# Kernel optimization log

Measured on AMD Instinct MI355X. Metric: run time of the kernel, lower is better.

## Reference

```python
import jax, jax.numpy as jnp
import numpy as np

B, D, N, H = 2, 8, 40, 128
HID = 4 * H  # 512, MLP hidden width


def setup_inputs() -> dict:
    key = jax.random.key(0)
    ks = jax.random.split(key, 12)
    s_in = 1.0 / np.sqrt(2 * H)
    s_hid = 1.0 / np.sqrt(HID)
    return {
        "node_feature": jax.random.normal(ks[0], (B, D, N, H), jnp.float32),
        "pairwise_feature": jax.random.normal(ks[1], (B, D, N, N, H), jnp.float32),
        # first MLP layer weight [2H, HID] split into node half and pairwise half
        "W1n": jax.random.uniform(ks[2], (H, HID), jnp.float32, -s_in, s_in),
        "W1p": jax.random.uniform(ks[3], (H, HID), jnp.float32, -s_in, s_in),
        "b1": jax.random.uniform(ks[4], (HID,), jnp.float32, -s_in, s_in),
        "W2": jax.random.uniform(ks[5], (HID, HID), jnp.float32, -s_hid, s_hid),
        "b2": jax.random.uniform(ks[6], (HID,), jnp.float32, -s_hid, s_hid),
        "W3": jax.random.uniform(ks[7], (HID, 1), jnp.float32, -s_hid, s_hid),
        "b3": jax.random.uniform(ks[8], (1,), jnp.float32, -s_hid, s_hid),
        "scale": jnp.float32(1.0),
        "bias": jnp.float32(0.0),
    }


def reference(node_feature, pairwise_feature, W1n, W1p, b1, W2, b2, W3, b3, scale, bias):
    # max over the dataset axis
    nf = jnp.max(node_feature, axis=-3)        # [B, N, H]
    pf = jnp.max(pairwise_feature, axis=-4)    # [B, N, N, H]
    # First linear on concat([node_expand, pair_expand]) decomposed into two
    # small projections + broadcast add (mathematically identical to
    # Linear(concat) since W1 = [W1n; W1p]).
    hn = nf @ W1n                               # [B, N, HID]
    hp = pf @ W1p                               # [B, N, N, HID]
    h = jax.nn.relu(hn[:, :, None, None, :] + hp[:, None, :, :, :] + b1)  # [B,N,N,N,HID]
    h = jax.nn.relu(h @ W2 + b2)                # [B, N, N, N, HID]
    v = h @ W3 + b3                             # [B, N, N, N, 1]
    return jax.nn.sigmoid(scale * v + bias).squeeze(-1)  # [B, N, N, N]
```

## Files before the change

kernel.cpp:

```cpp
#include <hip/hip_runtime.h>
#include <math.h>

#define BB 2
#define DD 8
#define NN 40
#define HH 128
#define HID 512
#define NJK 1600
#define MROW 64000

typedef __attribute__((ext_vector_type(8))) short short8;
typedef __attribute__((ext_vector_type(4))) float floatx4;

static __device__ __forceinline__ unsigned short f2bf(float x) {
    unsigned int b = __float_as_uint(x);
    b += 0x7fffu + ((b >> 16) & 1u);
    return (unsigned short)(b >> 16);
}

__global__ __launch_bounds__(256) void prep_kernel(
        const float* __restrict__ node, const float* __restrict__ pair,
        const float* __restrict__ W1n, const float* __restrict__ W1p,
        const float* __restrict__ b1, const float* __restrict__ W2,
        float* __restrict__ hp, float* __restrict__ hnb,
        unsigned short* __restrict__ w2f) {
    const int bid = blockIdx.x;
    const int t = threadIdx.x;

    if (bid < 200) {
        __shared__ float pf[16][HH];
        const int rowbase = bid * 16;
        for (int e = t; e < 16*HH; e += 256) {
            int r16 = e >> 7, c = e & 127;
            int grow = rowbase + r16;
            int b = grow / NJK, jk = grow - b*NJK;
            float m = -INFINITY;
            #pragma unroll
            for (int d = 0; d < DD; ++d)
                m = fmaxf(m, pair[((size_t)((b*DD + d)*NJK + jk))*HH + c]);
            pf[r16][c] = m;
        }
        __syncthreads();
        const int rg = t >> 7, c4 = (t & 127) * 4;
        float4 acc[8];
        #pragma unroll
        for (int r = 0; r < 8; ++r) acc[r] = make_float4(0.f,0.f,0.f,0.f);
        #pragma unroll 4
        for (int h = 0; h < HH; ++h) {
            float4 wv = *(const float4*)&W1p[h*HID + c4];
            #pragma unroll
            for (int r = 0; r < 8; ++r) {
                float pv = pf[rg*8 + r][h];
                acc[r].x = fmaf(pv, wv.x, acc[r].x);
                acc[r].y = fmaf(pv, wv.y, acc[r].y);
                acc[r].z = fmaf(pv, wv.z, acc[r].z);
                acc[r].w = fmaf(pv, wv.w, acc[r].w);
            }
        }
        #pragma unroll
        for (int r = 0; r < 8; ++r)
            *(float4*)&hp[(size_t)(rowbase + rg*8 + r)*HID + c4] = acc[r];
    } else if (bid < 205) {
        __shared__ float nf[16][HH];
        const int rowbase = (bid - 200) * 16;
        for (int e = t; e < 16*HH; e += 256) {
            int r16 = e >> 7, c = e & 127;
            int grow = rowbase + r16;
            int b = grow / NN, i = grow - b*NN;
            float m = -INFINITY;
            #pragma unroll
            for (int d = 0; d < DD; ++d)
                m = fmaxf(m, node[((size_t)((b*DD + d)*NN + i))*HH + c]);
            nf[r16][c] = m;
        }
        __syncthreads();
        const int rg = t >> 7, c4 = (t & 127) * 4;
        float4 acc[8];
        #pragma unroll
        for (int r = 0; r < 8; ++r) acc[r] = make_float4(0.f,0.f,0.f,0.f);
        #pragma unroll 4
        for (int h = 0; h < HH; ++h) {
            float4 wv = *(const float4*)&W1n[h*HID + c4];
            #pragma unroll
            for (int r = 0; r < 8; ++r) {
                float nv = nf[rg*8 + r][h];
                acc[r].x = fmaf(nv, wv.x, acc[r].x);
                acc[r].y = fmaf(nv, wv.y, acc[r].y);
                acc[r].z = fmaf(nv, wv.z, acc[r].z);
                acc[r].w = fmaf(nv, wv.w, acc[r].w);
            }
        }
        float4 b1v = *(const float4*)&b1[c4];
        #pragma unroll
        for (int r = 0; r < 8; ++r) {
            float4 o = make_float4(acc[r].x + b1v.x, acc[r].y + b1v.y,
                                   acc[r].z + b1v.z, acc[r].w + b1v.w);
            *(float4*)&hnb[(size_t)(rowbase + rg*8 + r)*HID + c4] = o;
        }
    } else {
        int tid = (bid - 205)*256 + t;
        int frag = tid >> 6;
        int lane = tid & 63;
        int n  = (frag >> 4)*16 + (lane & 15);
        int k0 = (frag & 15)*32 + (lane >> 4)*8;
        short8 u;
        #pragma unroll
        for (int kk = 0; kk < 8; ++kk)
            u[kk] = (short)f2bf(W2[(size_t)(k0 + kk)*HID + n]);
        *(short8*)(w2f + (size_t)tid*8) = u;
    }
}

__global__ __launch_bounds__(1024, 4) void main_kernel(
        const float* __restrict__ hp, const float* __restrict__ hnb,
        const unsigned short* __restrict__ w2f,
        const float* __restrict__ b2, const float* __restrict__ W3,
        const float* __restrict__ b3, const float* __restrict__ scale,
        const float* __restrict__ bias, float* __restrict__ out) {
    __shared__ unsigned short h1s[128 * HID];
    __shared__ float hnbs[8 * HID];
    __shared__ float red[8][128];

    const int bid  = blockIdx.x;
    const int bid8 = (bid & 7)*125 + (bid >> 3);
    const int b    = bid8 / 500;
    const int rr_  = bid8 % 500;
    const int i0   = (rr_ / 100) * 8;
    const int jk0  = (rr_ % 100) * 16;
    const int t    = threadIdx.x;
    char* h1c = (char*)h1s;

    {
        int row = t >> 7, c4 = (t & 127) * 4;
        *(float4*)&hnbs[row*HID + c4] =
            *(const float4*)&hnb[(size_t)(b*NN + i0 + row)*HID + c4];
    }
    __syncthreads();

    const float* hpb = hp + ((size_t)b*NJK + jk0)*HID;
    #pragma unroll
    for (int it = 0; it < 8; ++it) {
        int g   = it*1024 + t;
        int row = g >> 6, k8 = g & 63;
        int il  = row >> 4, jl = row & 15;
        const float* hr = hpb + (size_t)jl*HID + k8*8;
        const float* nr = hnbs + il*HID + k8*8;
        float4 p0 = *(const float4*)hr, p1 = *(const float4*)(hr + 4);
        float4 n0 = *(const float4*)nr, n1 = *(const float4*)(nr + 4);
        short8 u;
        u[0] = (short)f2bf(fmaxf(p0.x + n0.x, 0.f));
        u[1] = (short)f2bf(fmaxf(p0.y + n0.y, 0.f));
        u[2] = (short)f2bf(fmaxf(p0.z + n0.z, 0.f));
        u[3] = (short)f2bf(fmaxf(p0.w + n0.w, 0.f));
        u[4] = (short)f2bf(fmaxf(p1.x + n1.x, 0.f));
        u[5] = (short)f2bf(fmaxf(p1.y + n1.y, 0.f));
        u[6] = (short)f2bf(fmaxf(p1.z + n1.z, 0.f));
        u[7] = (short)f2bf(fmaxf(p1.w + n1.w, 0.f));
        int off = ((row << 10) + (k8 << 4)) ^ ((row & 7) << 4);
        *(short8*)(h1c + off) = u;
    }
    __syncthreads();

    const int w  = t >> 6, l = t & 63;
    const int rg = w >> 3, cw = w & 7;
    const int lr = l & 15, lg = l >> 4;

    floatx4 acc[4][4];
    #pragma unroll
    for (int mi = 0; mi < 4; ++mi)
        #pragma unroll
        for (int tn = 0; tn < 4; ++tn)
            acc[mi][tn] = (floatx4){0.f, 0.f, 0.f, 0.f};

    const unsigned short* bbase = w2f + (size_t)cw*32768 + l*8;
    const int rowb = rg*64 + lr;
    const int swz  = (lr & 7) << 4;

    #pragma unroll 1
    for (int ks = 0; ks < 16; ++ks) {
        short8 bf[4], av[4];
        #pragma unroll
        for (int tn = 0; tn < 4; ++tn)
            bf[tn] = *(const short8*)(bbase + ((tn*16 + ks) << 9));
        #pragma unroll
        for (int mi = 0; mi < 4; ++mi) {
            int aoff = (((rowb + mi*16) << 10) + (ks << 6) + (lg << 4)) ^ swz;
            av[mi] = *(const short8*)(h1c + aoff);
        }
        #pragma unroll
        for (int mi = 0; mi < 4; ++mi)
            #pragma unroll
            for (int tn = 0; tn < 4; ++tn)
                acc[mi][tn] = __builtin_amdgcn_mfma_f32_16x16x32_bf16(av[mi], bf[tn], acc[mi][tn], 0, 0, 0);
    }

    float b2v[4], w3v[4];
    #pragma unroll
    for (int tn = 0; tn < 4; ++tn) {
        int col = cw*64 + tn*16 + lr;
        b2v[tn] = b2[col];
        w3v[tn] = W3[col];
    }
    #pragma unroll
    for (int mi = 0; mi < 4; ++mi) {
        #pragma unroll
        for (int q = 0; q < 4; ++q) {
            float s = 0.f;
            #pragma unroll
            for (int tn = 0; tn < 4; ++tn)
                s += fmaxf(acc[mi][tn][q] + b2v[tn], 0.f) * w3v[tn];
            s += __shfl_xor(s, 1);
            s += __shfl_xor(s, 2);
            s += __shfl_xor(s, 4);
            s += __shfl_xor(s, 8);
            if (lr == 0) red[cw][rg*64 + mi*16 + lg*4 + q] = s;
        }
    }
    __syncthreads();
    if (t < 128) {
        float v = b3[0];
        #pragma unroll
        for (int c = 0; c < 8; ++c) v += red[c][t];
        float z = scale[0]*v + bias[0];
        int il = t >> 4, jl = t & 15;
        out[(size_t)b*MROW + (size_t)(i0 + il)*NJK + jk0 + jl] =
            1.0f / (1.0f + expf(-z));
    }
}

extern "C" void kernel_launch(void* const* d_in, const int* in_sizes, int n_in,
                              void* d_out, int out_size, void* d_ws, size_t ws_size,
                              hipStream_t stream) {
    const float* node  = (const float*)d_in[0];
    const float* pair  = (const float*)d_in[1];
    const float* W1n   = (const float*)d_in[2];
    const float* W1p   = (const float*)d_in[3];
    const float* b1    = (const float*)d_in[4];
    const float* W2    = (const float*)d_in[5];
    const float* b2    = (const float*)d_in[6];
    const float* W3    = (const float*)d_in[7];
    const float* b3    = (const float*)d_in[8];
    const float* scale = (const float*)d_in[9];
    const float* bias  = (const float*)d_in[10];
    float* out = (float*)d_out;

    float* hp = (float*)d_ws;
    float* hnb = hp + (size_t)BB*NJK*HID;
    unsigned short* w2f = (unsigned short*)(hnb + BB*NN*HID);

    hipLaunchKernelGGL(prep_kernel, dim3(333), dim3(256), 0, stream,
                       node, pair, W1n, W1p, b1, W2, hp, hnb, w2f);
    hipLaunchKernelGGL(main_kernel, dim3(1000), dim3(1024), 0, stream,
                       hp, hnb, w2f, b2, W3, b3, scale, bias, out);
}
```

Baseline: 184.8 us.

## Halve main block to 512 threads, widen per-wave M tile, prefetch W2 fragments

Main kernel now runs 8 waves per block, each computing all 128 rows against a 64-column slice of W2. This doubles A-fragment reuse per B load, and the next k-step's B fragments are prefetched into registers. The hnb staging in LDS is dropped in favour of direct global reads. The prep kernel now uses 8-row tiles (more blocks) and transposes W2 through padded shared memory for coalesced reads. Accumulator registers double (128 floats per lane), which can lower occupancy or cause spills.

```diff
diff --git a/kernel.cpp b/kernel.cpp
--- a/kernel.cpp
+++ b/kernel.cpp
@@ -24,33 +24,35 @@
         const float* __restrict__ b1, const float* __restrict__ W2,
         float* __restrict__ hp, float* __restrict__ hnb,
         unsigned short* __restrict__ w2f) {
+    __shared__ float smem[32 * 513];
     const int bid = blockIdx.x;
     const int t = threadIdx.x;
 
-    if (bid < 200) {
-        __shared__ float pf[16][HH];
-        const int rowbase = bid * 16;
-        for (int e = t; e < 16*HH; e += 256) {
-            int r16 = e >> 7, c = e & 127;
-            int grow = rowbase + r16;
+    if (bid < 400) {
+        float (*pf)[HH] = (float (*)[HH])smem;
+        const int rowbase = bid * 8;
+        #pragma unroll
+        for (int e = t; e < 8*HH; e += 256) {
+            int r8 = e >> 7, c = e & 127;
+            int grow = rowbase + r8;
             int b = grow / NJK, jk = grow - b*NJK;
             float m = -INFINITY;
             #pragma unroll
             for (int d = 0; d < DD; ++d)
                 m = fmaxf(m, pair[((size_t)((b*DD + d)*NJK + jk))*HH + c]);
-            pf[r16][c] = m;
+            pf[r8][c] = m;
         }
         __syncthreads();
         const int rg = t >> 7, c4 = (t & 127) * 4;
-        float4 acc[8];
-        #pragma unroll
-        for (int r = 0; r < 8; ++r) acc[r] = make_float4(0.f,0.f,0.f,0.f);
+        float4 acc[4];
+        #pragma unroll
+        for (int r = 0; r < 4; ++r) acc[r] = make_float4(0.f,0.f,0.f,0.f);
         #pragma unroll 4
         for (int h = 0; h < HH; ++h) {
             float4 wv = *(const float4*)&W1p[h*HID + c4];
             #pragma unroll
-            for (int r = 0; r < 8; ++r) {
-                float pv = pf[rg*8 + r][h];
+            for (int r = 0; r < 4; ++r) {
+                float pv = pf[rg*4 + r][h];
                 acc[r].x = fmaf(pv, wv.x, acc[r].x);
                 acc[r].y = fmaf(pv, wv.y, acc[r].y);
                 acc[r].z = fmaf(pv, wv.z, acc[r].z);
@@ -58,32 +60,33 @@
             }
         }
         #pragma unroll
-        for (int r = 0; r < 8; ++r)
-            *(float4*)&hp[(size_t)(rowbase + rg*8 + r)*HID + c4] = acc[r];
-    } else if (bid < 205) {
-        __shared__ float nf[16][HH];
-        const int rowbase = (bid - 200) * 16;
-        for (int e = t; e < 16*HH; e += 256) {
-            int r16 = e >> 7, c = e & 127;
-            int grow = rowbase + r16;
+        for (int r = 0; r < 4; ++r)
+            *(float4*)&hp[(size_t)(rowbase + rg*4 + r)*HID + c4] = acc[r];
+    } else if (bid < 410) {
+        float (*nf)[HH] = (float (*)[HH])smem;
+        const int rowbase = (bid - 400) * 8;
+        #pragma unroll
+        for (int e = t; e < 8*HH; e += 256) {
+            int r8 = e >> 7, c = e & 127;
+            int grow = rowbase + r8;
             int b = grow / NN, i = grow - b*NN;
             float m = -INFINITY;
             #pragma unroll
             for (int d = 0; d < DD; ++d)
                 m = fmaxf(m, node[((size_t)((b*DD + d)*NN + i))*HH + c]);
-            nf[r16][c] = m;
+            nf[r8][c] = m;
         }
         __syncthreads();
         const int rg = t >> 7, c4 = (t & 127) * 4;
-        float4 acc[8];
-        #pragma unroll
-        for (int r = 0; r < 8; ++r) acc[r] = make_float4(0.f,0.f,0.f,0.f);
+        float4 acc[4];
+        #pragma unroll
+        for (int r = 0; r < 4; ++r) acc[r] = make_float4(0.f,0.f,0.f,0.f);
         #pragma unroll 4
         for (int h = 0; h < HH; ++h) {
             float4 wv = *(const float4*)&W1n[h*HID + c4];
             #pragma unroll
-            for (int r = 0; r < 8; ++r) {
-                float nv = nf[rg*8 + r][h];
+            for (int r = 0; r < 4; ++r) {
+                float nv = nf[rg*4 + r][h];
                 acc[r].x = fmaf(nv, wv.x, acc[r].x);
                 acc[r].y = fmaf(nv, wv.y, acc[r].y);
                 acc[r].z = fmaf(nv, wv.z, acc[r].z);
@@ -92,33 +95,39 @@
         }
         float4 b1v = *(const float4*)&b1[c4];
         #pragma unroll
-        for (int r = 0; r < 8; ++r) {
+        for (int r = 0; r < 4; ++r) {
             float4 o = make_float4(acc[r].x + b1v.x, acc[r].y + b1v.y,
                                    acc[r].z + b1v.z, acc[r].w + b1v.w);
-            *(float4*)&hnb[(size_t)(rowbase + rg*8 + r)*HID + c4] = o;
+            *(float4*)&hnb[(size_t)(rowbase + rg*4 + r)*HID + c4] = o;
         }
     } else {
-        int tid = (bid - 205)*256 + t;
-        int frag = tid >> 6;
-        int lane = tid & 63;
-        int n  = (frag >> 4)*16 + (lane & 15);
-        int k0 = (frag & 15)*32 + (lane >> 4)*8;
-        short8 u;
-        #pragma unroll
-        for (int kk = 0; kk < 8; ++kk)
-            u[kk] = (short)f2bf(W2[(size_t)(k0 + kk)*HID + n]);
-        *(short8*)(w2f + (size_t)tid*8) = u;
-    }
-}
-
-__global__ __launch_bounds__(1024, 4) void main_kernel(
+        const int ks = bid - 410;
+        for (int e = t; e < 32*HID; e += 256) {
+            int r = e >> 9, c = e & 511;
+            smem[r*513 + c] = W2[(size_t)(ks*32 + r)*HID + c];
+        }
+        __syncthreads();
+        const int w = t >> 6, l = t & 63;
+        const int lr = l & 15, lg = l >> 4;
+        #pragma unroll
+        for (int f = 0; f < 8; ++f) {
+            int cf = w*8 + f;
+            short8 u;
+            #pragma unroll
+            for (int kk = 0; kk < 8; ++kk)
+                u[kk] = (short)f2bf(smem[(lg*8 + kk)*513 + cf*16 + lr]);
+            *(short8*)(w2f + (size_t)(cf*16 + ks)*512 + l*8) = u;
+        }
+    }
+}
+
+__global__ __launch_bounds__(512, 2) void main_kernel(
         const float* __restrict__ hp, const float* __restrict__ hnb,
         const unsigned short* __restrict__ w2f,
         const float* __restrict__ b2, const float* __restrict__ W3,
         const float* __restrict__ b3, const float* __restrict__ scale,
         const float* __restrict__ bias, float* __restrict__ out) {
     __shared__ unsigned short h1s[128 * HID];
-    __shared__ float hnbs[8 * HID];
     __shared__ float red[8][128];
 
     const int bid  = blockIdx.x;
@@ -130,21 +139,15 @@
     const int t    = threadIdx.x;
     char* h1c = (char*)h1s;
 
-    {
-        int row = t >> 7, c4 = (t & 127) * 4;
-        *(float4*)&hnbs[row*HID + c4] =
-            *(const float4*)&hnb[(size_t)(b*NN + i0 + row)*HID + c4];
-    }
-    __syncthreads();
-
-    const float* hpb = hp + ((size_t)b*NJK + jk0)*HID;
-    #pragma unroll
-    for (int it = 0; it < 8; ++it) {
-        int g   = it*1024 + t;
+    const float* hpb  = hp  + ((size_t)b*NJK + jk0)*HID;
+    const float* hnbb = hnb + ((size_t)(b*NN + i0))*HID;
+    #pragma unroll 4
+    for (int it = 0; it < 16; ++it) {
+        int g   = it*512 + t;
         int row = g >> 6, k8 = g & 63;
         int il  = row >> 4, jl = row & 15;
-        const float* hr = hpb + (size_t)jl*HID + k8*8;
-        const float* nr = hnbs + il*HID + k8*8;
+        const float* hr = hpb  + (size_t)jl*HID + k8*8;
+        const float* nr = hnbb + (size_t)il*HID + k8*8;
         float4 p0 = *(const float4*)hr, p1 = *(const float4*)(hr + 4);
         float4 n0 = *(const float4*)nr, n1 = *(const float4*)(nr + 4);
         short8 u;
@@ -162,47 +165,54 @@
     __syncthreads();
 
     const int w  = t >> 6, l = t & 63;
-    const int rg = w >> 3, cw = w & 7;
     const int lr = l & 15, lg = l >> 4;
-
-    floatx4 acc[4][4];
-    #pragma unroll
-    for (int mi = 0; mi < 4; ++mi)
+    const int swz = (lr & 7) << 4;
+
+    floatx4 acc[8][4];
+    #pragma unroll
+    for (int mi = 0; mi < 8; ++mi)
         #pragma unroll
         for (int tn = 0; tn < 4; ++tn)
             acc[mi][tn] = (floatx4){0.f, 0.f, 0.f, 0.f};
 
-    const unsigned short* bbase = w2f + (size_t)cw*32768 + l*8;
-    const int rowb = rg*64 + lr;
-    const int swz  = (lr & 7) << 4;
+    const unsigned short* bbase = w2f + (size_t)w*32768 + l*8;
+
+    short8 bcur[4];
+    #pragma unroll
+    for (int tn = 0; tn < 4; ++tn)
+        bcur[tn] = *(const short8*)(bbase + ((tn*16 + 0) << 9));
 
     #pragma unroll 1
     for (int ks = 0; ks < 16; ++ks) {
-        short8 bf[4], av[4];
+        short8 bnxt[4];
+        int ksn = (ks + 1) & 15;
         #pragma unroll
         for (int tn = 0; tn < 4; ++tn)
-            bf[tn] = *(const short8*)(bbase + ((tn*16 + ks) << 9));
-        #pragma unroll
-        for (int mi = 0; mi < 4; ++mi) {
-            int aoff = (((rowb + mi*16) << 10) + (ks << 6) + (lg << 4)) ^ swz;
+            bnxt[tn] = *(const short8*)(bbase + ((tn*16 + ksn) << 9));
+        short8 av[8];
+        #pragma unroll
+        for (int mi = 0; mi < 8; ++mi) {
+            int aoff = (((mi*16 + lr) << 10) + (ks << 6) + (lg << 4)) ^ swz;
             av[mi] = *(const short8*)(h1c + aoff);
         }
         #pragma unroll
-        for (int mi = 0; mi < 4; ++mi)
+        for (int mi = 0; mi < 8; ++mi)
             #pragma unroll
             for (int tn = 0; tn < 4; ++tn)
-                acc[mi][tn] = __builtin_amdgcn_mfma_f32_16x16x32_bf16(av[mi], bf[tn], acc[mi][tn], 0, 0, 0);
+                acc[mi][tn] = __builtin_amdgcn_mfma_f32_16x16x32_bf16(av[mi], bcur[tn], acc[mi][tn], 0, 0, 0);
+        #pragma unroll
+        for (int tn = 0; tn < 4; ++tn) bcur[tn] = bnxt[tn];
     }
 
     float b2v[4], w3v[4];
     #pragma unroll
     for (int tn = 0; tn < 4; ++tn) {
-        int col = cw*64 + tn*16 + lr;
+        int col = w*64 + tn*16 + lr;
         b2v[tn] = b2[col];
         w3v[tn] = W3[col];
     }
     #pragma unroll
-    for (int mi = 0; mi < 4; ++mi) {
+    for (int mi = 0; mi < 8; ++mi) {
         #pragma unroll
         for (int q = 0; q < 4; ++q) {
             float s = 0.f;
@@ -213,7 +223,7 @@
             s += __shfl_xor(s, 2);
             s += __shfl_xor(s, 4);
             s += __shfl_xor(s, 8);
-            if (lr == 0) red[cw][rg*64 + mi*16 + lg*4 + q] = s;
+            if (lr == 0) red[w][mi*16 + lg*4 + q] = s;
         }
     }
     __syncthreads();
@@ -248,8 +258,8 @@
     float* hnb = hp + (size_t)BB*NJK*HID;
     unsigned short* w2f = (unsigned short*)(hnb + BB*NN*HID);
 
-    hipLaunchKernelGGL(prep_kernel, dim3(333), dim3(256), 0, stream,
+    hipLaunchKernelGGL(prep_kernel, dim3(426), dim3(256), 0, stream,
                        node, pair, W1n, W1p, b1, W2, hp, hnb, w2f);
-    hipLaunchKernelGGL(main_kernel, dim3(1000), dim3(1024), 0, stream,
+    hipLaunchKernelGGL(main_kernel, dim3(1000), dim3(512), 0, stream,
                        hp, hnb, w2f, b2, W3, b3, scale, bias, out);
 }
```

Measured after the change: 179.5 us. -2.9%, faster.
